# Kernel tuning notes

Measured on AMD Instinct MI355X. Metric: run time of the kernel, lower is better.

## Reference

```python
import jax, jax.numpy as jnp
import numpy as np

ALPHA = 1.702  # GLU sigmoid scale
LIMIT = 7.0    # clamp limit
B, S, H, E, F, TOP_K = 2, 1024, 768, 16, 768, 4


def setup_inputs() -> dict:
    key = jax.random.key(0)
    ks = jax.random.split(key, 7)
    return {
        "hidden_states": jax.random.normal(ks[0], (B, S, H), jnp.float32),
        "router_weight": jax.random.normal(ks[1], (E, H), jnp.float32) * 0.02,
        "router_bias": jax.random.normal(ks[2], (E,), jnp.float32) * 0.02,
        "gate_up_proj": jax.random.normal(ks[3], (E, H, 2 * F), jnp.float32) * 0.02,
        "gate_up_proj_bias": jax.random.normal(ks[4], (E, 2 * F), jnp.float32) * 0.02,
        "down_proj": jax.random.normal(ks[5], (E, F, H), jnp.float32) * 0.02,
        "down_proj_bias": jax.random.normal(ks[6], (E, H), jnp.float32) * 0.02,
        "top_k": TOP_K,
    }


def reference(hidden_states, router_weight, router_bias, gate_up_proj,
              gate_up_proj_bias, down_proj, down_proj_bias, top_k):
    b, s, h = hidden_states.shape
    x = hidden_states.reshape(-1, h)                      # [T, H]
    t = x.shape[0]
    # ---- TopK router ----
    logits = x @ router_weight.T + router_bias            # [T, E]
    top_val, top_idx = jax.lax.top_k(logits, top_k)       # [T, K]
    top_val = jax.nn.softmax(top_val, axis=-1)
    router_scores = jnp.zeros_like(logits).at[
        jnp.arange(t)[:, None], top_idx].set(top_val)     # [T, E]
    # ---- Dense (all-expert) FFN, as in the reference repeat+bmm ----
    gate_up = jnp.einsum('th,ehf->etf', x, gate_up_proj) \
        + gate_up_proj_bias[:, None, :]                   # [E, T, 2F]
    gate = jnp.minimum(gate_up[..., 0::2], LIMIT)         # clamp(max=limit)
    up = jnp.clip(gate_up[..., 1::2], -LIMIT, LIMIT)
    glu = gate * jax.nn.sigmoid(gate * ALPHA)
    expert_out = jnp.einsum('etf,efh->eth', (up + 1.0) * glu, down_proj) \
        + down_proj_bias[:, None, :]                      # [E, T, H]
    expert_out = expert_out.reshape(-1, b, s, h)          # [E, B, S, H]
    w = router_scores.T.reshape(-1, b, s)[..., None]      # [E, B, S, 1]
    routed_out = (expert_out * w).sum(axis=0)             # [B, S, H]
    return routed_out, router_scores
```

## Files before the change

### kernel.cpp

```cpp
#include <hip/hip_runtime.h>
#include <hip/hip_bf16.h>

#define T_TOK 2048
#define H_DIM 768
#define E_NUM 16
#define F_DIM 768
#define TWOF 1536
#define TOPK 4
#define NASSIGN 8192
#define BM 128
#define BK 64
#define KT 12
#define NTILE 80
#define NSLOTP (NTILE * BM)
#define MAXT1 10
#define CHUNK (BM * BK)
#define WTILE (64 * BK)
#define NRTR 256

typedef __bf16 bf16x8 __attribute__((ext_vector_type(8)));
typedef unsigned short us8 __attribute__((ext_vector_type(8)));
typedef float f32x4 __attribute__((ext_vector_type(4)));

__device__ __forceinline__ unsigned short f2bf(float f) {
  unsigned u = __float_as_uint(f);
  u += 0x7FFF + ((u >> 16) & 1);
  return (unsigned short)(u >> 16);
}

__device__ __forceinline__ void gl_lds16(const unsigned short* g, unsigned short* l) {
  __builtin_amdgcn_global_load_lds(
      (const __attribute__((address_space(1))) unsigned int*)g,
      (__attribute__((address_space(3))) unsigned int*)l, 16, 0, 0);
}

__global__ __launch_bounds__(256)
void router_kernel(const float* __restrict__ x, const float* __restrict__ rw,
                   const float* __restrict__ rb, float* __restrict__ scores,
                   int* __restrict__ tk_idx, float* __restrict__ tk_w,
                   int* __restrict__ tmap, float* __restrict__ wgrp) {
  __shared__ float lg[8][16], sc[8][16];
  const int bid = blockIdx.x;
  const int tid = threadIdx.x;
  const int t0 = bid * 8;
  if (tid < 40) {
    tmap[bid * 40 + tid] = 0;
    wgrp[bid * 40 + tid] = 0.0f;
  }
  const int lane32 = tid & 31, tok = tid >> 5;
  const int e = lane32 & 15, q2 = lane32 >> 4;
  const int t = t0 + tok;
  const float* xr = x + (size_t)t * H_DIM + q2 * 384;
  const float* wr = rw + (size_t)e * H_DIM + q2 * 384;
  double a0 = 0, a1 = 0, a2 = 0, a3 = 0;
  #pragma unroll 4
  for (int h = 0; h < 384; h += 4) {
    const f32x4 xv = *(const f32x4*)(xr + h);
    const f32x4 wv = *(const f32x4*)(wr + h);
    a0 += (double)xv[0] * (double)wv[0];
    a1 += (double)xv[1] * (double)wv[1];
    a2 += (double)xv[2] * (double)wv[2];
    a3 += (double)xv[3] * (double)wv[3];
  }
  double acc = (a0 + a1) + (a2 + a3);
  acc += __shfl_xor(acc, 16, 64);
  if (q2 == 0) lg[tok][e] = (float)acc + rb[e];
  __syncthreads();
  if (lane32 == 0) {
    float v[16];
    #pragma unroll
    for (int i = 0; i < 16; ++i) { v[i] = lg[tok][i]; sc[tok][i] = 0.0f; }
    int idx[TOPK]; float val[TOPK];
    for (int k = 0; k < TOPK; ++k) {
      float best = -3.4e38f; int bi = 0;
      for (int i = 0; i < 16; ++i)
        if (v[i] > best) { best = v[i]; bi = i; }
      idx[k] = bi; val[k] = best; v[bi] = -3.4e38f;
    }
    float s = 0.0f, ev[TOPK];
    for (int k = 0; k < TOPK; ++k) { ev[k] = expf(val[k] - val[0]); s += ev[k]; }
    for (int k = 0; k < TOPK; ++k) {
      float wgt = ev[k] / s;
      sc[tok][idx[k]] = wgt;
      tk_idx[t * TOPK + k] = idx[k];
      tk_w[t * TOPK + k] = wgt;
    }
  }
  __syncthreads();
  if (tid < 128)
    scores[(size_t)(t0 + (tid >> 4)) * 16 + (tid & 15)] = sc[tid >> 4][tid & 15];
}

__global__ __launch_bounds__(256)
void group_kernel(const int* __restrict__ tk_idx, const float* __restrict__ tk_w,
                  int* __restrict__ counts, int* __restrict__ offs,
                  int* __restrict__ tmap, float* __restrict__ wgrp) {
  __shared__ int hist[256][16];
  __shared__ int seg[16][16];
  __shared__ int cnt[16], eoff[16];
  const int tid = threadIdx.x;
  int loc[16];
  #pragma unroll
  for (int e = 0; e < 16; ++e) loc[e] = 0;
  const int base = tid * 32;
  int eid[32];
  for (int i = 0; i < 32; ++i) { int e = tk_idx[base + i]; eid[i] = e; loc[e]++; }
  #pragma unroll
  for (int e = 0; e < 16; ++e) hist[tid][e] = loc[e];
  __syncthreads();
  const int s = tid >> 4, e16 = tid & 15;
  {
    int sum = 0;
    #pragma unroll
    for (int j = 0; j < 16; ++j) sum += hist[s * 16 + j][e16];
    seg[s][e16] = sum;
  }
  __syncthreads();
  if (tid < 16) {
    int run = 0;
    #pragma unroll
    for (int s2 = 0; s2 < 16; ++s2) { int t = seg[s2][tid]; seg[s2][tid] = run; run += t; }
    cnt[tid] = run;
  }
  __syncthreads();
  {
    int run = seg[s][e16];
    #pragma unroll
    for (int j = 0; j < 16; ++j) { int t = hist[s * 16 + j][e16]; hist[s * 16 + j][e16] = run; run += t; }
  }
  __syncthreads();
  if (tid == 0) {
    int acc = 0;
    for (int e = 0; e < 16; ++e) { eoff[e] = acc; acc += (cnt[e] + BM - 1) / BM * BM; }
  }
  __syncthreads();
  if (tid < 16) { counts[tid] = cnt[tid]; offs[tid] = eoff[tid]; }
  int run[16];
  #pragma unroll
  for (int e = 0; e < 16; ++e) run[e] = hist[tid][e];
  for (int i = 0; i < 32; ++i) {
    int e = eid[i];
    int slot = eoff[e] + run[e]++;
    tmap[slot] = base + i;
    wgrp[slot] = tk_w[base + i];
  }
}

__global__ __launch_bounds__(512)
void convert_w_kernel(const float* __restrict__ gup, const float* __restrict__ dwn,
                      unsigned short* __restrict__ gw, unsigned short* __restrict__ uw,
                      unsigned short* __restrict__ dw) {
  const int ft = blockIdx.x, kt = blockIdx.y, z = blockIdx.z;
  const int tid = threadIdx.x;
  const int n = tid & 63, k8 = tid >> 6;
  const int doff = n * BK + 8 * (k8 ^ (n & 7));
  __shared__ unsigned short tg[WTILE], tu[WTILE];
  if (z < 16) {
    const int e = z;
    const float* src = gup + ((size_t)(e * H_DIM + kt * 64 + k8 * 8)) * TWOF
                           + 2 * (ft * 64 + n);
    us8 g, u;
    #pragma unroll
    for (int j = 0; j < 8; ++j) {
      const float2 p = *(const float2*)(src + (size_t)j * TWOF);
      g[j] = f2bf(p.x); u[j] = f2bf(p.y);
    }
    *(us8*)&tg[doff] = g;
    *(us8*)&tu[doff] = u;
    __syncthreads();
    const size_t tb = (((size_t)e * KT + kt) * 12 + ft) * WTILE;
    *(us8*)&gw[tb + tid * 8] = *(const us8*)&tg[tid * 8];
    *(us8*)&uw[tb + tid * 8] = *(const us8*)&tu[tid * 8];
  } else {
    const int e = z - 16;
    const float* src = dwn + ((size_t)(e * F_DIM + kt * 64 + k8 * 8)) * H_DIM
                           + ft * 64 + n;
    us8 o;
    #pragma unroll
    for (int j = 0; j < 8; ++j) o[j] = f2bf(src[(size_t)j * H_DIM]);
    *(us8*)&tg[doff] = o;
    __syncthreads();
    const size_t tb = (((size_t)e * KT + kt) * 12 + ft) * WTILE;
    *(us8*)&dw[tb + tid * 8] = *(const us8*)&tg[tid * 8];
  }
}

__global__ __launch_bounds__(256)
void convert_x_kernel(const float* __restrict__ x, const int* __restrict__ tmap,
                      unsigned short* __restrict__ xg) {
  const int tile = blockIdx.x;
  const int kt = blockIdx.y;
  const int tid = threadIdx.x;
  const int r = tid >> 1;
  const int c0 = (tid & 1) * 32;
  const int tok = tmap[tile * BM + r] >> 2;
  const float* src = x + (size_t)tok * H_DIM + kt * 64 + c0;
  unsigned short* dst = xg + ((size_t)tile * KT + kt) * CHUNK + r * BK;
  #pragma unroll
  for (int qq = 0; qq < 4; ++qq) {
    f32x4 a = *(const f32x4*)(src + 8 * qq);
    f32x4 b = *(const f32x4*)(src + 8 * qq + 4);
    us8 o;
    #pragma unroll
    for (int j = 0; j < 4; ++j) { o[j] = f2bf(a[j]); o[4+j] = f2bf(b[j]); }
    const int k8 = (c0 >> 3) + qq;
    *(us8*)&dst[8 * (k8 ^ (r & 7))] = o;
  }
}

__global__ __launch_bounds__(512)
void gemm1_kernel(const unsigned short* __restrict__ xg, const unsigned short* __restrict__ gw,
                  const unsigned short* __restrict__ uw, const float* __restrict__ gupb,
                  const int* __restrict__ counts, const int* __restrict__ offs,
                  unsigned short* __restrict__ act) {
  const int bid = blockIdx.x;
  const int swz = (bid & 7) * 120 + (bid >> 3);
  const int ey = swz / 6, ft = swz % 6;
  const int e = ey / MAXT1, tile = ey % MAXT1;
  const int count = counts[e];
  if (tile * BM >= count) return;
  const int tileg = (offs[e] >> 7) + tile;
  const int tid = threadIdx.x;
  const int wv = tid >> 6, lane = tid & 63;
  const int ml = lane & 15, lh = lane >> 4;
  const int wm = wv >> 2, wn = wv & 3;

  __shared__ unsigned short lA[CHUNK];
  __shared__ unsigned short lBg[CHUNK];
  __shared__ unsigned short lBu[CHUNK];

  const unsigned short* ab = xg + (size_t)tileg * KT * CHUNK;
  const unsigned short* gb = gw + ((size_t)e * KT * 12 + ft * 2) * WTILE;
  const unsigned short* ub = uw + ((size_t)e * KT * 12 + ft * 2) * WTILE;

  f32x4 accg[4][2] = {};
  f32x4 accu[4][2] = {};

  for (int kt = 0; kt < KT; ++kt) {
    const unsigned short* as = ab + kt * CHUNK;
    const unsigned short* gs = gb + (size_t)kt * 12 * WTILE;
    const unsigned short* us = ub + (size_t)kt * 12 * WTILE;
    gl_lds16(as + tid * 8, &lA[tid * 8]);
    gl_lds16(as + (512 + tid) * 8, &lA[(512 + tid) * 8]);
    gl_lds16(gs + tid * 8, &lBg[tid * 8]);
    gl_lds16(gs + (512 + tid) * 8, &lBg[(512 + tid) * 8]);
    gl_lds16(us + tid * 8, &lBu[tid * 8]);
    gl_lds16(us + (512 + tid) * 8, &lBu[(512 + tid) * 8]);
    __syncthreads();
    #pragma unroll
    for (int ks = 0; ks < 2; ++ks) {
      const int slot = ks * 4 + lh;
      bf16x8 af[4];
      #pragma unroll
      for (int mf = 0; mf < 4; ++mf) {
        const int ar = wm * 64 + mf * 16 + ml;
        af[mf] = __builtin_bit_cast(bf16x8, *(const us8*)&lA[ar * BK + 8 * (slot ^ (ar & 7))]);
      }
      #pragma unroll
      for (int nf = 0; nf < 2; ++nf) {
        const int br = wn * 32 + nf * 16 + ml;
        const int ba = (br >> 6) * WTILE + (br & 63) * BK + 8 * (slot ^ (br & 7));
        bf16x8 bg = __builtin_bit_cast(bf16x8, *(const us8*)&lBg[ba]);
        bf16x8 bu = __builtin_bit_cast(bf16x8, *(const us8*)&lBu[ba]);
        #pragma unroll
        for (int mf = 0; mf < 4; ++mf) {
          accg[mf][nf] = __builtin_amdgcn_mfma_f32_16x16x32_bf16(af[mf], bg, accg[mf][nf], 0, 0, 0);
          accu[mf][nf] = __builtin_amdgcn_mfma_f32_16x16x32_bf16(af[mf], bu, accu[mf][nf], 0, 0, 0);
        }
      }
    }
    __syncthreads();
  }
  unsigned short* tbuf = (wn & 2) ? lBg : lA;
  #pragma unroll
  for (int mf = 0; mf < 4; ++mf) {
    #pragma unroll
    for (int nf = 0; nf < 2; ++nf) {
      const int fcl = wn * 32 + nf * 16 + ml;
      const int c = fcl & 63;
      const int fc = ft * 128 + fcl;
      const float bgv = gupb[(size_t)e * TWOF + 2 * fc];
      const float buv = gupb[(size_t)e * TWOF + 2 * fc + 1];
      #pragma unroll
      for (int r = 0; r < 4; ++r) {
        const int m = wm * 64 + mf * 16 + lh * 4 + r;
        float g = accg[mf][nf][r] + bgv;
        float u = accu[mf][nf][r] + buv;
        g = fminf(g, 7.0f);
        u = fminf(fmaxf(u, -7.0f), 7.0f);
        const float glu = g / (1.0f + __expf(-1.702f * g));
        tbuf[m * BK + 8 * ((c >> 3) ^ (m & 7)) + (c & 7)] = f2bf((u + 1.0f) * glu);
      }
    }
  }
  __syncthreads();
  unsigned short* ob0 = act + ((size_t)tileg * KT + ft * 2) * CHUNK;
  unsigned short* ob1 = ob0 + CHUNK;
  #pragma unroll
  for (int i = 0; i < 2; ++i) {
    *(us8*)&ob0[(i * 512 + tid) * 8] = *(const us8*)&lA[(i * 512 + tid) * 8];
    *(us8*)&ob1[(i * 512 + tid) * 8] = *(const us8*)&lBg[(i * 512 + tid) * 8];
  }
}

__global__ __launch_bounds__(512)
void gemm2_kernel(const unsigned short* __restrict__ act, const unsigned short* __restrict__ dw,
                  const float* __restrict__ dwnb, const int* __restrict__ counts,
                  const int* __restrict__ offs, const int* __restrict__ tmap,
                  const float* __restrict__ wgrp, float* __restrict__ partial) {
  const int bid = blockIdx.x;
  const int swz = (bid & 7) * 120 + (bid >> 3);
  const int ey = swz / 6, ft = swz % 6;
  const int e = ey / MAXT1, tile = ey % MAXT1;
  const int count = counts[e];
  if (tile * BM >= count) return;
  const int off = offs[e];
  const int tileg = (off >> 7) + tile;
  const int tid = threadIdx.x;
  const int wv = tid >> 6, lane = tid & 63;
  const int ml = lane & 15, lh = lane >> 4;
  const int wm = wv >> 2, wn = wv & 3;

  __shared__ unsigned short lA[CHUNK];
  __shared__ unsigned short lB[CHUNK];

  const unsigned short* ab = act + (size_t)tileg * KT * CHUNK;
  const unsigned short* bb = dw + ((size_t)e * KT * 12 + ft * 2) * WTILE;

  f32x4 acc[4][2] = {};

  for (int kt = 0; kt < KT; ++kt) {
    const unsigned short* as = ab + kt * CHUNK;
    const unsigned short* bs = bb + (size_t)kt * 12 * WTILE;
    gl_lds16(as + tid * 8, &lA[tid * 8]);
    gl_lds16(as + (512 + tid) * 8, &lA[(512 + tid) * 8]);
    gl_lds16(bs + tid * 8, &lB[tid * 8]);
    gl_lds16(bs + (512 + tid) * 8, &lB[(512 + tid) * 8]);
    __syncthreads();
    #pragma unroll
    for (int ks = 0; ks < 2; ++ks) {
      const int slot = ks * 4 + lh;
      bf16x8 af[4];
      #pragma unroll
      for (int mf = 0; mf < 4; ++mf) {
        const int ar = wm * 64 + mf * 16 + ml;
        af[mf] = __builtin_bit_cast(bf16x8, *(const us8*)&lA[ar * BK + 8 * (slot ^ (ar & 7))]);
      }
      #pragma unroll
      for (int nf = 0; nf < 2; ++nf) {
        const int br = wn * 32 + nf * 16 + ml;
        const int ba = (br >> 6) * WTILE + (br & 63) * BK + 8 * (slot ^ (br & 7));
        bf16x8 bv = __builtin_bit_cast(bf16x8, *(const us8*)&lB[ba]);
        #pragma unroll
        for (int mf = 0; mf < 4; ++mf)
          acc[mf][nf] = __builtin_amdgcn_mfma_f32_16x16x32_bf16(af[mf], bv, acc[mf][nf], 0, 0, 0);
      }
    }
    __syncthreads();
  }
  #pragma unroll
  for (int mf = 0; mf < 4; ++mf) {
    #pragma unroll
    for (int nf = 0; nf < 2; ++nf) {
      const int hc = ft * 128 + wn * 32 + nf * 16 + ml;
      const float bias = dwnb[(size_t)e * H_DIM + hc];
      #pragma unroll
      for (int r = 0; r < 4; ++r) {
        const int m = tile * BM + wm * 64 + mf * 16 + lh * 4 + r;
        if (m < count) {
          const int slot = off + m;
          partial[(size_t)tmap[slot] * H_DIM + hc] = wgrp[slot] * (acc[mf][nf][r] + bias);
        }
      }
    }
  }
}

__global__ __launch_bounds__(256)
void reduce_kernel(const float* __restrict__ partial, float* __restrict__ out) {
  const int idx = blockIdx.x * 256 + threadIdx.x;
  const int v = idx * 4;
  const int t = v / H_DIM;
  const int h = v - t * H_DIM;
  f32x4 s = {0, 0, 0, 0};
  #pragma unroll
  for (int k = 0; k < 4; ++k) {
    const f32x4 p = *(const f32x4*)&partial[(size_t)(t * 4 + k) * H_DIM + h];
    s += p;
  }
  *(f32x4*)&out[v] = s;
}

extern "C" void kernel_launch(void* const* d_in, const int* in_sizes, int n_in,
                              void* d_out, int out_size, void* d_ws, size_t ws_size,
                              hipStream_t stream) {
  const float* x    = (const float*)d_in[0];
  const float* rw   = (const float*)d_in[1];
  const float* rb   = (const float*)d_in[2];
  const float* gup  = (const float*)d_in[3];
  const float* gupb = (const float*)d_in[4];
  const float* dwn  = (const float*)d_in[5];
  const float* dwnb = (const float*)d_in[6];
  float* out = (float*)d_out;
  float* scores = out + (size_t)T_TOK * H_DIM;

  char* w = (char*)d_ws;
  int*   tk_idx = (int*)w;            w += NASSIGN * 4;
  float* tk_w   = (float*)w;          w += NASSIGN * 4;
  int*   counts = (int*)w;            w += 64;
  int*   offs   = (int*)w;            w += 64;
  int*   tmap   = (int*)w;            w += NSLOTP * 4;
  float* wgrp   = (float*)w;          w += NSLOTP * 4;
  unsigned short* gw = (unsigned short*)w; w += (size_t)E_NUM * KT * 12 * WTILE * 2;
  unsigned short* uw = (unsigned short*)w; w += (size_t)E_NUM * KT * 12 * WTILE * 2;
  unsigned short* dw = (unsigned short*)w; w += (size_t)E_NUM * KT * 12 * WTILE * 2;
  unsigned short* xg = (unsigned short*)w; w += (size_t)NTILE * KT * CHUNK * 2;
  unsigned short* act = (unsigned short*)w; w += (size_t)NTILE * KT * CHUNK * 2;
  float* partial = (float*)w;         w += (size_t)NASSIGN * H_DIM * 4;

  convert_w_kernel<<<dim3(12, 12, 32), 512, 0, stream>>>(gup, dwn, gw, uw, dw);
  router_kernel<<<NRTR, 256, 0, stream>>>(x, rw, rb, scores, tk_idx, tk_w, tmap, wgrp);
  group_kernel<<<1, 256, 0, stream>>>(tk_idx, tk_w, counts, offs, tmap, wgrp);
  convert_x_kernel<<<dim3(NTILE, KT), 256, 0, stream>>>(x, tmap, xg);
  gemm1_kernel<<<6 * E_NUM * MAXT1, 512, 0, stream>>>(
      xg, gw, uw, gupb, counts, offs, act);
  gemm2_kernel<<<6 * E_NUM * MAXT1, 512, 0, stream>>>(
      act, dw, dwnb, counts, offs, tmap, wgrp, partial);
  reduce_kernel<<<(T_TOK * H_DIM / 4) / 256, 256, 0, stream>>>(partial, out);
}
```

Measured before the change: 126.0 us.

## Fuse x bf16 conversion into router and gather rows directly in gemm1

The separate convert_x kernel, which gathered and converted token rows into per-tile swizzled chunks, is removed. The router kernel now converts x to bf16 in plain token-major layout. gemm1 uses tmap to gather each A row straight from that buffer with global_load_lds, applying the XOR swizzle through the source column offset. This drops one kernel launch and the 4x duplicated write of gathered x, at the cost of scattered row reads inside the GEMM.

Result: faster. 117.0 us (-7.2%).

```diff
diff --git a/kernel.cpp b/kernel.cpp
--- a/kernel.cpp
+++ b/kernel.cpp
@@ -38,7 +38,8 @@
 void router_kernel(const float* __restrict__ x, const float* __restrict__ rw,
                    const float* __restrict__ rb, float* __restrict__ scores,
                    int* __restrict__ tk_idx, float* __restrict__ tk_w,
-                   int* __restrict__ tmap, float* __restrict__ wgrp) {
+                   int* __restrict__ tmap, float* __restrict__ wgrp,
+                   unsigned short* __restrict__ xg) {
   __shared__ float lg[8][16], sc[8][16];
   const int bid = blockIdx.x;
   const int tid = threadIdx.x;
@@ -46,6 +47,22 @@
   if (tid < 40) {
     tmap[bid * 40 + tid] = 0;
     wgrp[bid * 40 + tid] = 0.0f;
+  }
+  {
+    const int tokr = tid >> 5;
+    const int g0 = tid & 31;
+    const float* xs = x + (size_t)(t0 + tokr) * H_DIM;
+    unsigned short* xd = xg + (size_t)(t0 + tokr) * H_DIM;
+    #pragma unroll
+    for (int i = 0; i < 3; ++i) {
+      const int gg = g0 + i * 32;
+      const f32x4 a = *(const f32x4*)(xs + gg * 8);
+      const f32x4 b = *(const f32x4*)(xs + gg * 8 + 4);
+      us8 o;
+      #pragma unroll
+      for (int j = 0; j < 4; ++j) { o[j] = f2bf(a[j]); o[4 + j] = f2bf(b[j]); }
+      *(us8*)&xd[gg * 8] = o;
+    }
   }
   const int lane32 = tid & 31, tok = tid >> 5;
   const int e = lane32 & 15, q2 = lane32 >> 4;
@@ -185,34 +202,11 @@
   }
 }
 
-__global__ __launch_bounds__(256)
-void convert_x_kernel(const float* __restrict__ x, const int* __restrict__ tmap,
-                      unsigned short* __restrict__ xg) {
-  const int tile = blockIdx.x;
-  const int kt = blockIdx.y;
-  const int tid = threadIdx.x;
-  const int r = tid >> 1;
-  const int c0 = (tid & 1) * 32;
-  const int tok = tmap[tile * BM + r] >> 2;
-  const float* src = x + (size_t)tok * H_DIM + kt * 64 + c0;
-  unsigned short* dst = xg + ((size_t)tile * KT + kt) * CHUNK + r * BK;
-  #pragma unroll
-  for (int qq = 0; qq < 4; ++qq) {
-    f32x4 a = *(const f32x4*)(src + 8 * qq);
-    f32x4 b = *(const f32x4*)(src + 8 * qq + 4);
-    us8 o;
-    #pragma unroll
-    for (int j = 0; j < 4; ++j) { o[j] = f2bf(a[j]); o[4+j] = f2bf(b[j]); }
-    const int k8 = (c0 >> 3) + qq;
-    *(us8*)&dst[8 * (k8 ^ (r & 7))] = o;
-  }
-}
-
 __global__ __launch_bounds__(512)
 void gemm1_kernel(const unsigned short* __restrict__ xg, const unsigned short* __restrict__ gw,
                   const unsigned short* __restrict__ uw, const float* __restrict__ gupb,
                   const int* __restrict__ counts, const int* __restrict__ offs,
-                  unsigned short* __restrict__ act) {
+                  const int* __restrict__ tmap, unsigned short* __restrict__ act) {
   const int bid = blockIdx.x;
   const int swz = (bid & 7) * 120 + (bid >> 3);
   const int ey = swz / 6, ft = swz % 6;
@@ -229,7 +223,13 @@
   __shared__ unsigned short lBg[CHUNK];
   __shared__ unsigned short lBu[CHUNK];
 
-  const unsigned short* ab = xg + (size_t)tileg * KT * CHUNK;
+  const int arow = tid >> 3;
+  const int agr = (tid & 7) ^ (arow & 7);
+  const int t0 = tmap[tileg * BM + arow] >> 2;
+  const int t1 = tmap[tileg * BM + 64 + arow] >> 2;
+  const unsigned short* a0 = xg + (size_t)t0 * H_DIM + agr * 8;
+  const unsigned short* a1 = xg + (size_t)t1 * H_DIM + agr * 8;
+
   const unsigned short* gb = gw + ((size_t)e * KT * 12 + ft * 2) * WTILE;
   const unsigned short* ub = uw + ((size_t)e * KT * 12 + ft * 2) * WTILE;
 
@@ -237,11 +237,10 @@
   f32x4 accu[4][2] = {};
 
   for (int kt = 0; kt < KT; ++kt) {
-    const unsigned short* as = ab + kt * CHUNK;
     const unsigned short* gs = gb + (size_t)kt * 12 * WTILE;
     const unsigned short* us = ub + (size_t)kt * 12 * WTILE;
-    gl_lds16(as + tid * 8, &lA[tid * 8]);
-    gl_lds16(as + (512 + tid) * 8, &lA[(512 + tid) * 8]);
+    gl_lds16(a0 + kt * 64, &lA[tid * 8]);
+    gl_lds16(a1 + kt * 64, &lA[(512 + tid) * 8]);
     gl_lds16(gs + tid * 8, &lBg[tid * 8]);
     gl_lds16(gs + (512 + tid) * 8, &lBg[(512 + tid) * 8]);
     gl_lds16(us + tid * 8, &lBu[tid * 8]);
@@ -414,16 +413,15 @@
   unsigned short* gw = (unsigned short*)w; w += (size_t)E_NUM * KT * 12 * WTILE * 2;
   unsigned short* uw = (unsigned short*)w; w += (size_t)E_NUM * KT * 12 * WTILE * 2;
   unsigned short* dw = (unsigned short*)w; w += (size_t)E_NUM * KT * 12 * WTILE * 2;
-  unsigned short* xg = (unsigned short*)w; w += (size_t)NTILE * KT * CHUNK * 2;
+  unsigned short* xg = (unsigned short*)w; w += (size_t)T_TOK * H_DIM * 2;
   unsigned short* act = (unsigned short*)w; w += (size_t)NTILE * KT * CHUNK * 2;
   float* partial = (float*)w;         w += (size_t)NASSIGN * H_DIM * 4;
 
   convert_w_kernel<<<dim3(12, 12, 32), 512, 0, stream>>>(gup, dwn, gw, uw, dw);
-  router_kernel<<<NRTR, 256, 0, stream>>>(x, rw, rb, scores, tk_idx, tk_w, tmap, wgrp);
+  router_kernel<<<NRTR, 256, 0, stream>>>(x, rw, rb, scores, tk_idx, tk_w, tmap, wgrp, xg);
   group_kernel<<<1, 256, 0, stream>>>(tk_idx, tk_w, counts, offs, tmap, wgrp);
-  convert_x_kernel<<<dim3(NTILE, KT), 256, 0, stream>>>(x, tmap, xg);
   gemm1_kernel<<<6 * E_NUM * MAXT1, 512, 0, stream>>>(
-      xg, gw, uw, gupb, counts, offs, act);
+      xg, gw, uw, gupb, counts, offs, tmap, act);
   gemm2_kernel<<<6 * E_NUM * MAXT1, 512, 0, stream>>>(
       act, dw, dwnb, counts, offs, tmap, wgrp, partial);
   reduce_kernel<<<(T_TOK * H_DIM / 4) / 256, 256, 0, stream>>>(partial, out);
```
